# Performance work log

Measured on AMD Instinct MI355X. Metric: run time of the kernel, lower is better.

## Reference

```python
import jax, jax.numpy as jnp
import numpy as np

N, G, E, HD, H, L = 22528, 1024, 473088, 64, 4, 4
C = HD  # per-head out channels; concat=False -> mean over heads


def _ln(x, g, b, eps=1e-5):
    m = x.mean(-1, keepdims=True)
    v = ((x - m) ** 2).mean(-1, keepdims=True)
    return (x - m) * jax.lax.rsqrt(v + eps) * g + b


def setup_inputs() -> dict:
    key = jax.random.key(0)
    ks = iter(jax.random.split(key, 48))
    def rn(shape, s=0.1):
        return jax.random.normal(next(ks), shape, jnp.float32) * s
    inp = {}
    inp['x'] = jax.random.normal(next(ks), (N, 7), jnp.float32)
    inp['edge_index'] = jax.random.randint(next(ks), (2, E), 0, N)
    inp['edge_attr'] = jax.random.normal(next(ks), (E, 5), jnp.float32)
    inp['context'] = jax.random.normal(next(ks), (G, 3), jnp.float32)
    inp['batch'] = jnp.sort(jax.random.randint(next(ks), (N,), 0, G))
    inp['role'] = jax.random.randint(next(ks), (N,), 0, 5)
    inp['side'] = jax.random.randint(next(ks), (N,), 0, 3)
    inp['formation'] = jax.random.randint(next(ks), (G,), 0, 8)
    inp['alignment'] = jax.random.randint(next(ks), (G,), 0, 10)
    inp.update(
        W_emb=rn((7, HD)), b_emb=jnp.zeros((HD,)),
        role_table=rn((5, HD)), side_table=rn((3, HD // 2)),
        W_ctx=rn((3, HD)), b_ctx=jnp.zeros((HD,)),
        form_table=rn((8, HD)), align_table=rn((10, HD)),
        Wl=rn((L, HD, H * C)), bl=jnp.zeros((L, H * C)),
        Wr=rn((L, HD, H * C)), br=jnp.zeros((L, H * C)),
        We=rn((L, 5, H * C)), att=rn((L, H, C)), gat_bias=jnp.zeros((L, C)),
        ln_g=jnp.ones((L, HD)), ln_b=jnp.zeros((L, HD)),
        sp_W1=rn((2 * HD, HD)), sp_b1=jnp.zeros((HD,)),
        sp_W2=rn((HD, HD)), sp_b2=jnp.zeros((HD,)),
        sp_Wg=rn((HD, HD)), sp_bg=jnp.zeros((HD,)),
        fn_g=jnp.ones((HD,)), fn_b=jnp.zeros((HD,)),
    )
    return inp


def reference(x, edge_index, edge_attr, context, batch, role, side, formation, alignment,
              W_emb, b_emb, role_table, side_table, W_ctx, b_ctx, form_table, align_table,
              Wl, bl, Wr, br, We, att, gat_bias, ln_g, ln_b,
              sp_W1, sp_b1, sp_W2, sp_b2, sp_Wg, sp_bg, fn_g, fn_b):
    n = x.shape[0]
    # input embedding + categorical embedding fusion
    h = jax.nn.relu(x @ W_emb + b_emb)
    h = h + role_table[role]
    s = side_table[side]
    h = h + jnp.pad(s, ((0, 0), (0, h.shape[1] - s.shape[1])))
    c = jax.nn.relu(context @ W_ctx + b_ctx) + form_table[formation] + align_table[alignment]
    h = h + c[batch]
    src, dst = edge_index[0], edge_index[1]
    # PyG GATv2Conv default add_self_loops=True, fill_value='mean' for edge_attr
    deg_in = jax.ops.segment_sum(jnp.ones((src.shape[0], 1), h.dtype), dst, num_segments=n)
    self_attr = jax.ops.segment_sum(edge_attr, dst, num_segments=n) / jnp.maximum(deg_in, 1.0)
    loop = jnp.arange(n)
    src_a = jnp.concatenate([src, loop])
    dst_a = jnp.concatenate([dst, loop])
    ea = jnp.concatenate([edge_attr, self_attr], axis=0)
    for i in range(Wl.shape[0]):
        h_res = h
        x_l = (h @ Wl[i] + bl[i]).reshape(n, H, C)
        x_r = (h @ Wr[i] + br[i]).reshape(n, H, C)
        ee = (ea @ We[i]).reshape(-1, H, C)
        e = jax.nn.leaky_relu(x_l[src_a] + x_r[dst_a] + ee, 0.2)  # [E', H, C]
        logits = jnp.einsum('ehc,hc->eh', e, att[i])
        m = jax.lax.stop_gradient(jax.ops.segment_max(logits, dst_a, num_segments=n))
        p = jnp.exp(logits - m[dst_a])
        denom = jax.ops.segment_sum(p, dst_a, num_segments=n)
        alpha = p / denom[dst_a]  # softmax over incoming edges per head
        out = jax.ops.segment_sum(alpha[:, :, None] * x_l[src_a], dst_a, num_segments=n)
        out = out.mean(axis=1) + gat_bias[i]  # concat=False -> head mean + bias
        h = _ln(jax.nn.relu(out) + h_res, ln_g[i], ln_b[i])
    # social pooling: gated pairwise MLP, scatter-mean onto src
    pair = jnp.concatenate([h[src], h[dst]], axis=-1)
    inter = jax.nn.relu(pair @ sp_W1 + sp_b1) @ sp_W2 + sp_b2
    gated = inter * jax.nn.sigmoid(inter @ sp_Wg + sp_bg)
    cnt = jax.ops.segment_sum(jnp.ones((src.shape[0], 1), h.dtype), src, num_segments=n)
    pooled = jax.ops.segment_sum(gated, src, num_segments=n) / jnp.maximum(cnt, 1.0)
    h = h + pooled
    return _ln(h, fn_g, fn_b)
```

## Files before the change

kernel.cpp:

```cpp
#include <hip/hip_runtime.h>
#include <hip/hip_bf16.h>
#include <hip/hip_fp16.h>

#define N_NODES 22528
#define N_GRAPH 1024
#define N_EDGE  473088
#define HD 64

typedef unsigned short u16;
typedef unsigned int u32;
typedef unsigned char u8;
typedef __attribute__((ext_vector_type(8))) short bf16x8;
typedef __attribute__((ext_vector_type(4))) float f32x4;
typedef __attribute__((ext_vector_type(2))) float f32x2;
typedef __attribute__((ext_vector_type(4))) unsigned int u32x4;
typedef __attribute__((ext_vector_type(2))) _Float16 h2;
typedef __attribute__((ext_vector_type(2))) __fp16 fp16x2;
typedef __attribute__((ext_vector_type(8))) __fp16 fp16x8;

union FragU { bf16x8 v; u16 u[8]; u32 w[4]; };
union Frag16 { fp16x8 v; u16 u[8]; u32 w[4]; };
union HbU { uint4 v; u16 u[8]; };
union EaU { uint4 v; u32x4 e; u16 u[8]; u32 w[4]; };
union H2U { u32 w; h2 h; fp16x2 f; };

__device__ __forceinline__ float b2f(u16 u) {
    union { u32 i; float f; } v; v.i = ((u32)u) << 16; return v.f;
}
__device__ __forceinline__ float lo16(u32 w) {
    union { u32 i; float f; } v; v.i = w << 16; return v.f;
}
__device__ __forceinline__ float hi16(u32 w) {
    union { u32 i; float f; } v; v.i = w & 0xFFFF0000u; return v.f;
}
__device__ __forceinline__ u16 f2b(float f) {
    union { float f; u32 i; } v; v.f = f;
    u32 u = v.i;
    return (u16)((u + 0x7FFFu + ((u >> 16) & 1u)) >> 16);
}
__device__ __forceinline__ u16 f2h(float f) {
    union { __half h; u16 u; } c; c.h = __float2half(f); return c.u;
}
__device__ __forceinline__ float hlo(u32 w) {
    union { u16 u; __half h; } c; c.u = (u16)(w & 0xFFFFu); return __half2float(c.h);
}
__device__ __forceinline__ float hhi(u32 w) {
    union { u16 u; __half h; } c; c.u = (u16)(w >> 16); return __half2float(c.h);
}
__device__ __forceinline__ u8 f2fp8(float f) {
    return (u8)(__builtin_amdgcn_cvt_pk_fp8_f32(f, f, 0, false) & 0xFF);
}
__device__ __forceinline__ void dec8(u32 w, float* x) {
    f32x2 lo = __builtin_amdgcn_cvt_pk_f32_fp8((int)w, false);
    f32x2 hi = __builtin_amdgcn_cvt_pk_f32_fp8((int)w, true);
    x[0] = lo.x; x[1] = lo.y; x[2] = hi.x; x[3] = hi.y;
}
__device__ __forceinline__ int rdfl(u32 v) { return __builtin_amdgcn_readfirstlane((int)v); }
__device__ __forceinline__ h2 sblo(u32 w) { H2U c; c.w = (w & 0xFFFFu) | (w << 16); return c.h; }
__device__ __forceinline__ h2 sbhi(u32 w) { H2U c; c.w = (w >> 16) | (w & 0xFFFF0000u); return c.h; }
__device__ __forceinline__ h2 pkh(float a, float b) {
    H2U c; c.f = __builtin_amdgcn_cvt_pkrtz(a, b); return c.h;
}
__device__ __forceinline__ h2 u32h2(u32 w) { H2U c; c.w = w; return c.h; }
__device__ __forceinline__ u32 h2u32(h2 x) { H2U c; c.h = x; return c.w; }

#if __has_builtin(__builtin_amdgcn_fdot2)
__device__ __forceinline__ float FDOT2(h2 a, h2 b, float c) { return __builtin_amdgcn_fdot2(a, b, c, false); }
#else
__device__ __forceinline__ float FDOT2(h2 a, h2 b, float c) {
    return c + (float)a[0] * (float)b[0] + (float)a[1] * (float)b[1];
}
#endif

__device__ __forceinline__ float sum16(float v) {
    v += __int_as_float(__builtin_amdgcn_update_dpp(0, __float_as_int(v), 0x121, 0xF, 0xF, true));
    v += __int_as_float(__builtin_amdgcn_update_dpp(0, __float_as_int(v), 0x122, 0xF, 0xF, true));
    v += __int_as_float(__builtin_amdgcn_update_dpp(0, __float_as_int(v), 0x124, 0xF, 0xF, true));
    v += __int_as_float(__builtin_amdgcn_update_dpp(0, __float_as_int(v), 0x128, 0xF, 0xF, true));
    return v;
}

#define N_CVT 27
struct CvtTab { const void* src[N_CVT]; float* dst[N_CVT]; int n[N_CVT]; };

#define CPB 2048
#define NCHUNK (N_EDGE / CPB)
#define NRANGE 8
#define NPR (N_NODES / NRANGE)

__global__ __launch_bounds__(256) void k_count(const int* ei, int* ddst, int* dsrc,
                                               const void* ln_g, int* flag) {
    if (blockIdx.x == 0 && threadIdx.x == 0) {
        u32 w = ((const u32*)ln_g)[0];
        *flag = (w == 0x3F800000u) ? 1 : 0;
    }
    int r = blockIdx.x & 7;
    int c = blockIdx.x >> 3;
    int rlo = r * NPR, rhi = rlo + NPR;
    int base = c * CPB + threadIdx.x;
#pragma unroll
    for (int j = 0; j < CPB / 256; j++) {
        int e = base + j * 256;
        int s = __builtin_nontemporal_load(ei + e);
        int d = __builtin_nontemporal_load(ei + N_EDGE + e);
        if (d >= rlo && d < rhi) atomicAdd(&ddst[d], 1);
        if (s >= rlo && s < rhi) atomicAdd(&dsrc[s], 1);
    }
}

__global__ __launch_bounds__(256) void k_convert(CvtTab tab, const int* flagp) {
    int ty = blockIdx.y;
    const void* s = tab.src[ty];
    float* d = tab.dst[ty];
    int n = tab.n[ty];
    int f = *flagp;
    int stride = gridDim.x * 256;
    int i0 = blockIdx.x * 256 + threadIdx.x;
    if (f) {
        const float* sf = (const float*)s;
        for (int i = i0; i < n; i += stride) d[i] = sf[i];
    } else {
        const u16* sb = (const u16*)s;
        for (int i = i0; i < n; i += stride) d[i] = b2f(sb[i]);
    }
}

__global__ __launch_bounds__(256) void k_prepwlr(const float* Wl, const float* Wr, u16* wflr) {
    int idx = blockIdx.x * 256 + threadIdx.x;
    int f = idx >> 6, lane = idx & 63;
    int layer = f >> 6, lr = (f >> 5) & 1, ct = (f >> 1) & 15, kt = f & 1;
    const float* W = (lr ? Wr : Wl) + (size_t)layer * 64 * 256;
    int q = lane >> 4, m = lane & 15;
#pragma unroll
    for (int j = 0; j < 8; j++) {
        int k = kt * 32 + q * 8 + j;
        int nn = ct * 16 + m;
        wflr[(size_t)f * 512 + lane * 8 + j] = f2b(W[k * 256 + nn]);
    }
}

#define SCB 44
__global__ __launch_bounds__(512) void k_scanA(const int* ddst, const int* dsrc,
                                               int* pos_dst, int* pos_src,
                                               int* partial_d, int* partial_s) {
    __shared__ int wd[8], wss[8], wdx[8], wsx[8];
    int tid = threadIdx.x;
    int lane = tid & 63, wv = tid >> 6;
    int i = blockIdx.x * 512 + tid;
    int dd = ddst[i] + 1;
    int ds = dsrc[i];
    int sd = dd, ss = ds;
#pragma unroll
    for (int o = 1; o < 64; o <<= 1) {
        int t0 = __shfl_up(sd, o, 64);
        int t1 = __shfl_up(ss, o, 64);
        if (lane >= o) { sd += t0; ss += t1; }
    }
    if (lane == 63) { wd[wv] = sd; wss[wv] = ss; }
    __syncthreads();
    if (tid == 0) {
        int cd = 0, cs = 0;
#pragma unroll
        for (int w = 0; w < 8; w++) {
            int td = wd[w], ts = wss[w];
            wdx[w] = cd; wsx[w] = cs;
            cd += td; cs += ts;
        }
        partial_d[blockIdx.x] = cd;
        partial_s[blockIdx.x] = cs;
    }
    __syncthreads();
    pos_dst[i] = wdx[wv] + sd - dd;
    pos_src[i] = wsx[wv] + ss - ds;
}

__global__ __launch_bounds__(128) void k_scanB(int* partial_d, int* partial_s,
                                               int* off_dst, int* off_src) {
    int tid = threadIdx.x;
    int lane = tid & 63, wv = tid >> 6;
    int* arr = wv ? partial_s : partial_d;
    int v = (lane < SCB) ? arr[lane] : 0;
    int s = v;
#pragma unroll
    for (int o = 1; o < 64; o <<= 1) {
        int t = __shfl_up(s, o, 64);
        if (lane >= o) s += t;
    }
    if (lane < SCB) arr[lane] = s - v;
    if (lane == SCB - 1) {
        if (wv) off_src[N_NODES] = s;
        else    off_dst[N_NODES] = s;
    }
}

__global__ __launch_bounds__(512) void k_scanC(const int* partial_d, const int* partial_s,
                                               int* off_dst, int* pos_dst,
                                               int* off_src, int* pos_src,
                                               int* selfpos) {
    int i = blockIdx.x * 512 + threadIdx.x;
    int bd = partial_d[blockIdx.x];
    int bs = partial_s[blockIdx.x];
    int v = bd + pos_dst[i];
    off_dst[i] = v;
    selfpos[i] = v;
    pos_dst[i] = v + 1;
    int vs = bs + pos_src[i];
    off_src[i] = vs;
    pos_src[i] = vs;
}

__global__ __launch_bounds__(256) void k_scatter(const int* ei, const void* eattr_raw, const int* flagp,
                                                 int* pos_dst, int* pos_src,
                                                 u16* epermb, int* dstp) {
    int r = blockIdx.x & 7;
    int c = blockIdx.x >> 3;
    int rlo = r * NPR, rhi = rlo + NPR;
    int f = *flagp;
    int base = c * CPB + threadIdx.x;
#pragma unroll
    for (int j = 0; j < CPB / 256; j++) {
        int e = base + j * 256;
        int s = __builtin_nontemporal_load(ei + e);
        int d = __builtin_nontemporal_load(ei + N_EDGE + e);
        if (d >= rlo && d < rhi) {
            EaU b;
#pragma unroll
            for (int k = 0; k < 8; k++) b.u[k] = 0;
            if (f) {
                const float* sf = (const float*)eattr_raw;
#pragma unroll
                for (int k = 0; k < 5; k++) b.u[k] = f2h(__builtin_nontemporal_load(sf + (size_t)e * 5 + k));
            } else {
                const u16* sb = (const u16*)eattr_raw;
#pragma unroll
                for (int k = 0; k < 5; k++) b.u[k] = f2h(b2f(__builtin_nontemporal_load(sb + (size_t)e * 5 + k)));
            }
            b.w[3] = (u32)s;
            int slot = atomicAdd(&pos_dst[d], 1);
            ((u32x4*)epermb)[slot] = b.e;
        }
        if (s >= rlo && s < rhi) {
            int slot2 = atomicAdd(&pos_src[s], 1);
            dstp[slot2] = d;
        }
    }
}

__global__ __launch_bounds__(256) void k_selfattr(const int* off_dst, const int* selfpos, u16* epermb) {
    int lane = threadIdx.x & 63, wv = threadIdx.x >> 6;
    int q = lane >> 4, m15 = lane & 15;
    int n = blockIdx.x * 16 + wv * 4 + q;
    int slot = selfpos[n];
    int e0 = off_dst[n], e1 = off_dst[n + 1];
    float s0 = 0.f, s1 = 0.f, s2 = 0.f, s3 = 0.f, s4 = 0.f;
    for (int ii = e0 + m15; ii < e1; ii += 16) {
        if (ii == slot) continue;
        uint4 w = ((const uint4*)epermb)[ii];
        s0 += hlo(w.x); s1 += hhi(w.x); s2 += hlo(w.y); s3 += hhi(w.y); s4 += hlo(w.z);
    }
    s0 = sum16(s0); s1 = sum16(s1); s2 = sum16(s2); s3 = sum16(s3); s4 = sum16(s4);
    if (m15 == 0) {
        float inv = 1.f / fmaxf((float)(e1 - e0 - 1), 1.f);
        EaU b;
#pragma unroll
        for (int k = 0; k < 8; k++) b.u[k] = 0;
        b.u[0] = f2h(s0 * inv); b.u[1] = f2h(s1 * inv); b.u[2] = f2h(s2 * inv);
        b.u[3] = f2h(s3 * inv); b.u[4] = f2h(s4 * inv);
        b.w[3] = (u32)n;
        ((uint4*)epermb)[slot] = b.v;
    }
}

__global__ __launch_bounds__(256) void k_embed(const float* x, const float* W_emb, const float* b_emb,
                                               const int* role, const int* side, const int* batch,
                                               const float* role_t, const float* side_t,
                                               const float* context, const int* formation, const int* alignment,
                                               const float* W_ctx, const float* b_ctx,
                                               const float* form_t, const float* align_t,
                                               float* h) {
    int lane = threadIdx.x & 63, wv = threadIdx.x >> 6;
    int n = blockIdx.x * 4 + wv;
    float a = b_emb[lane];
#pragma unroll
    for (int k = 0; k < 7; k++) a += x[n * 7 + k] * W_emb[k * 64 + lane];
    a = fmaxf(a, 0.f);
    a += role_t[role[n] * 64 + lane];
    if (lane < 32) a += side_t[side[n] * 32 + lane];
    int g = batch[n];
    float c = b_ctx[lane];
#pragma unroll
    for (int k = 0; k < 3; k++) c += context[g * 3 + k] * W_ctx[k * 64 + lane];
    c = fmaxf(c, 0.f);
    c += form_t[formation[g] * 64 + lane] + align_t[alignment[g] * 64 + lane];
    h[n * 64 + lane] = a + c;
}

#define ATS 72

__global__ __launch_bounds__(256) void k_xlxr(const float* h, const u16* wflrL,
                                              const float* bl, const float* br, u8* xl8, u16* xrb) {
    __shared__ u16 hs[16 * ATS];
    int t = threadIdx.x;
    int n0 = blockIdx.x * 16;
#pragma unroll
    for (int r = 0; r < 4; r++) {
        int idx = t + r * 256;
        int m = idx >> 6, k = idx & 63;
        hs[m * ATS + k] = f2b(h[(size_t)(n0 + m) * 64 + k]);
    }
    __syncthreads();
    int lane = t & 63, wv = t >> 6;
    int q = lane >> 4, m15 = lane & 15;
    bf16x8 a0 = *(const bf16x8*)(hs + m15 * ATS + q * 8);
    bf16x8 a1 = *(const bf16x8*)(hs + m15 * ATS + 32 + q * 8);
#pragma unroll
    for (int lr = 0; lr < 2; lr++) {
        const float* bias = lr ? br : bl;
#pragma unroll
        for (int c4 = 0; c4 < 4; c4++) {
            int ct = wv * 4 + c4;
            const u16* fb = wflrL + (size_t)((lr * 16 + ct) * 2) * 512;
            f32x4 c = (f32x4){0.f, 0.f, 0.f, 0.f};
            c = __builtin_amdgcn_mfma_f32_16x16x32_bf16(a0, *(const bf16x8*)(fb + lane * 8), c, 0, 0, 0);
            c = __builtin_amdgcn_mfma_f32_16x16x32_bf16(a1, *(const bf16x8*)(fb + 512 + lane * 8), c, 0, 0, 0);
            float b = bias[ct * 16 + m15];
#pragma unroll
            for (int reg = 0; reg < 4; reg++) {
                int row = q * 4 + reg;
                float v = c[reg] + b;
                if (lr) xrb[(size_t)(n0 + row) * 256 + ct * 16 + m15] = f2b(v);
                else    xl8[(size_t)(n0 + row) * 256 + ct * 16 + m15] = f2fp8(v);
            }
        }
    }
}

__global__ __launch_bounds__(256) void k_gat(const u8* __restrict__ xl8, const u16* __restrict__ xrb,
                                             const uint4* __restrict__ epermb, const int* __restrict__ off_dst,
                                             const float* __restrict__ We, const float* __restrict__ att,
                                             const float* __restrict__ gat_bias,
                                             const float* __restrict__ ln_g, const float* __restrict__ ln_b,
                                             float* __restrict__ h) {
    __shared__ float lacc[2][2][4][64];
    __shared__ float lsum[2][2][4];
    int t = threadIdx.x;
    int lane = t & 63, wv = t >> 6;
    int nl = wv >> 1, half = wv & 1;
    int n = blockIdx.x * 2 + nl;
    int q = lane >> 4, m15 = lane & 15;
    float4 a4 = ((const float4*)att)[lane];
    h2 attP0 = pkh(a4.x, a4.y),               attP1 = pkh(a4.z, a4.w);
    h2 attN0 = pkh(0.2f * a4.x, 0.2f * a4.y), attN1 = pkh(0.2f * a4.z, 0.2f * a4.w);
    h2 weh[5][2];
#pragma unroll
    for (int k = 0; k < 5; k++) {
        float4 w4 = ((const float4*)(We + k * 256))[lane];
        weh[k][0] = pkh(w4.x, w4.y);
        weh[k][1] = pkh(w4.z, w4.w);
    }
    ushort4 xrp = ((const ushort4*)xrb)[(size_t)n * 64 + lane];
    h2 xrh0 = pkh(b2f(xrp.x), b2f(xrp.y));
    h2 xrh1 = pkh(b2f(xrp.z), b2f(xrp.w));
    const h2 hz = {(_Float16)0.f, (_Float16)0.f};
    int e0 = rdfl((u32)off_dst[n]);
    int e1 = rdfl((u32)off_dst[n + 1]);
    int mid = e0 + ((e1 - e0 + 1) >> 1);
    int a0 = half ? mid : e0;
    int a1 = half ? e1 : mid;
    float s_own = 0.f;
    float acc[4] = {0.f, 0.f, 0.f, 0.f};
    const u32* xl32 = (const u32*)xl8;
    int ii = a0;
    for (; ii + 2 <= a1; ii += 2) {
        uint4 ew0 = epermb[ii];
        uint4 ew1 = epermb[ii + 1];
        int s0 = rdfl(ew0.w);
        int s1 = rdfl(ew1.w);
        u32 xw0 = xl32[(size_t)s0 * 64 + lane];
        u32 xw1 = xl32[(size_t)s1 * 64 + lane];
        u32 e0x = (u32)rdfl(ew0.x), e0y = (u32)rdfl(ew0.y), e0z = (u32)rdfl(ew0.z);
        u32 e1x = (u32)rdfl(ew1.x), e1y = (u32)rdfl(ew1.y), e1z = (u32)rdfl(ew1.z);
        h2 eA0 = sblo(e0x), eA1 = sbhi(e0x), eA2 = sblo(e0y), eA3 = sbhi(e0y), eA4 = sblo(e0z);
        h2 eB0 = sblo(e1x), eB1 = sbhi(e1x), eB2 = sblo(e1y), eB3 = sbhi(e1y), eB4 = sblo(e1z);
        float xlf0[4], xlf1[4];
        dec8(xw0, xlf0);
        dec8(xw1, xlf1);
        h2 x0a = pkh(xlf0[0], xlf0[1]), x0b = pkh(xlf0[2], xlf0[3]);
        h2 x1a = pkh(xlf1[0], xlf1[1]), x1b = pkh(xlf1[2], xlf1[3]);
        h2 v0a = x0a + xrh0;
        h2 v0b = x0b + xrh1;
        h2 v1a = x1a + xrh0;
        h2 v1b = x1b + xrh1;
        v0a += eA0 * weh[0][0]; v0b += eA0 * weh[0][1];
        v0a += eA1 * weh[1][0]; v0b += eA1 * weh[1][1];
        v0a += eA2 * weh[2][0]; v0b += eA2 * weh[2][1];
        v0a += eA3 * weh[3][0]; v0b += eA3 * weh[3][1];
        v0a += eA4 * weh[4][0]; v0b += eA4 * weh[4][1];
        h2 p0a = __builtin_elementwise_max(v0a, hz), m0a = __builtin_elementwise_min(v0a, hz);
        h2 p0b = __builtin_elementwise_max(v0b, hz), m0b = __builtin_elementwise_min(v0b, hz);
        h2 p1a = __builtin_elementwise_max(v1a, hz), m1a = __builtin_elementwise_min(v1a, hz);
        h2 p1b = __builtin_elementwise_max(v1b, hz), m1b = __builtin_elementwise_min(v1b, hz);
        float lp0 = FDOT2(p0a, attP0, 0.f);
        lp0 = FDOT2(m0a, attN0, lp0);
        lp0 = FDOT2(p0b, attP1, lp0);
        lp0 = FDOT2(m0b, attN1, lp0);
        float lp1 = FDOT2(p1a, attP0, 0.f);
        lp1 = FDOT2(m1a, attN0, lp1);
        lp1 = FDOT2(p1b, attP1, lp1);
        lp1 = FDOT2(m1b, attN1, lp1);
        lp0 = sum16(lp0);
        lp1 = sum16(lp1);
        float p0 = __expf(fminf(lp0, 50.f));
        float p1 = __expf(fminf(lp1, 50.f));
        s_own += p0 + p1;
        acc[0] += p0 * xlf0[0] + p1 * xlf1[0];
        acc[1] += p0 * xlf0[1] + p1 * xlf1[1];
        acc[2] += p0 * xlf0[2] + p1 * xlf1[2];
        acc[3] += p0 * xlf0[3] + p1 * xlf1[3];
    }
    if (ii < a1) {
        uint4 ew = epermb[ii];
        int s0 = rdfl(ew.w);
        u32 xw = xl32[(size_t)s0 * 64 + lane];
        u32 ex = (u32)rdfl(ew.x), ey = (u32)rdfl(ew.y), ez = (u32)rdfl(ew.z);
        h2 eA0 = sblo(ex), eA1 = sbhi(ex), eA2 = sblo(ey), eA3 = sbhi(ey), eA4 = sblo(ez);
        float xlf[4];
        dec8(xw, xlf);
        h2 xa = pkh(xlf[0], xlf[1]), xb = pkh(xlf[2], xlf[3]);
        h2 va = xa + xrh0;
        h2 vb = xb + xrh1;
        va += eA0 * weh[0][0]; vb += eA0 * weh[0][1];
        va += eA1 * weh[1][0]; vb += eA1 * weh[1][1];
        va += eA2 * weh[2][0]; vb += eA2 * weh[2][1];
        va += eA3 * weh[3][0]; vb += eA3 * weh[3][1];
        va += eA4 * weh[4][0]; vb += eA4 * weh[4][1];
        h2 pa = __builtin_elementwise_max(va, hz), ma = __builtin_elementwise_min(va, hz);
        h2 pb = __builtin_elementwise_max(vb, hz), mb = __builtin_elementwise_min(vb, hz);
        float lp = FDOT2(pa, attP0, 0.f);
        lp = FDOT2(ma, attN0, lp);
        lp = FDOT2(pb, attP1, lp);
        lp = FDOT2(mb, attN1, lp);
        lp = sum16(lp);
        float p = __expf(fminf(lp, 50.f));
        s_own += p;
        acc[0] += p * xlf[0]; acc[1] += p * xlf[1];
        acc[2] += p * xlf[2]; acc[3] += p * xlf[3];
    }
    *(float4*)&lacc[nl][half][q][m15 * 4] = make_float4(acc[0], acc[1], acc[2], acc[3]);
    if (m15 == 0) lsum[nl][half][q] = s_own;
    __syncthreads();
    if (half == 0) {
        float o = 0.f;
#pragma unroll
        for (int j = 0; j < 4; j++) {
            float sj = lsum[nl][0][j] + lsum[nl][1][j];
            float aj = lacc[nl][0][j][lane] + lacc[nl][1][j][lane];
            o += aj / sj;
        }
        o = 0.25f * o + gat_bias[lane];
        float r = fmaxf(o, 0.f) + h[(size_t)n * 64 + lane];
        float mu = r;
#pragma unroll
        for (int mask = 1; mask < 64; mask <<= 1) mu += __shfl_xor(mu, mask, 64);
        mu *= (1.f / 64.f);
        float d = r - mu;
        float var = d * d;
#pragma unroll
        for (int mask = 1; mask < 64; mask <<= 1) var += __shfl_xor(var, mask, 64);
        var *= (1.f / 64.f);
        h[(size_t)n * 64 + lane] = d * rsqrtf(var + 1e-5f) * ln_g[lane] + ln_b[lane];
    }
}

__global__ __launch_bounds__(256) void k_poolprep(const float* h, const float* W1, const float* sp_b1,
                                                  u16* hA, u16* hBb,
                                                  const float* W2, const float* Wg, u16* wfrag) {
    int t = threadIdx.x;
    if (blockIdx.x == N_NODES / 8) {
#pragma unroll
        for (int r = 0; r < 4; r++) {
            int i = t + r * 256;
            int frag = i >> 6, lane = i & 63;
            const float* W = (frag < 8) ? W2 : Wg;
            int f = frag & 7;
            int ct = f >> 1, kt = f & 1;
#pragma unroll
            for (int j = 0; j < 8; j++) {
                int k = kt * 32 + (lane >> 4) * 8 + j;
                int nn = ct * 16 + (lane & 15);
                wfrag[i * 8 + j] = f2h(W[k * 64 + nn]);
            }
        }
        return;
    }
    __shared__ float hs[512];
    int n0 = blockIdx.x * 8;
    hs[t] = h[n0 * 64 + t];
    hs[t + 256] = h[n0 * 64 + 256 + t];
    __syncthreads();
    int c = t & 63;
    int half = (t >> 6) & 1;
    int jg = t >> 7;
    const float* w = W1 + half * 4096;
    float acc[4] = {0.f, 0.f, 0.f, 0.f};
    for (int k = 0; k < 64; k++) {
        float wv_ = w[k * 64 + c];
#pragma unroll
        for (int j = 0; j < 4; j++) acc[j] += hs[(jg * 4 + j) * 64 + k] * wv_;
    }
    float b1 = sp_b1[c];
#pragma unroll
    for (int j = 0; j < 4; j++) {
        int n = n0 + jg * 4 + j;
        if (half) hBb[(size_t)n * 64 + c] = f2h(acc[j]);
        else      hA[(size_t)n * 64 + c] = f2h(acc[j] + b1);
    }
}

#define TBS 72

__global__ __launch_bounds__(256) void k_pool(const float* h, const u16* hA, const u16* hBb,
                                              const int* dstp, const int* off_src, const u16* wfrag,
                                              const float* sp_b2, const float* sp_bg,
                                              const float* fn_g, const float* fn_b,
                                              void* outv, const int* flagp) {
    __shared__ u16 smem[8192 + 4 * 16 * TBS];
    int t = threadIdx.x;
#pragma unroll
    for (int r = 0; r < 4; r++)
        ((uint4*)smem)[t + r * 256] = ((const uint4*)wfrag)[t + r * 256];
    __syncthreads();
    int lane = t & 63, wv = t >> 6;
    int n = blockIdx.x * 4 + wv;
    int q = lane >> 4, m15 = lane & 15;
    u16* tb = smem + 8192 + wv * 16 * TBS;

    const uint4* hap = (const uint4*)(hA + (size_t)n * 64);
    uint4 ha0r = hap[q], ha1r = hap[4 + q];
    h2 ha0h[4] = {u32h2(ha0r.x), u32h2(ha0r.y), u32h2(ha0r.z), u32h2(ha0r.w)};
    h2 ha1h[4] = {u32h2(ha1r.x), u32h2(ha1r.y), u32h2(ha1r.z), u32h2(ha1r.w)};
    const h2 hz = {(_Float16)0.f, (_Float16)0.f};
    float b2r[4], bgr[4];
#pragma unroll
    for (int ct = 0; ct < 4; ct++) {
        b2r[ct] = sp_b2[ct * 16 + m15];
        bgr[ct] = sp_bg[ct * 16 + m15];
    }
    f32x4 pacc[4];
#pragma unroll
    for (int ct = 0; ct < 4; ct++) pacc[ct] = (f32x4){0.f, 0.f, 0.f, 0.f};

    int e0 = off_src[n], e1 = off_src[n + 1];
    int deg = e1 - e0;
    for (int base = e0; base < e1; base += 16) {
        int slot = base + m15;
        int ec = (slot < e1) ? slot : (e1 - 1);
        int dst = dstp[ec];
        const uint4* hbp = (const uint4*)(hBb + (size_t)dst * 64);
        uint4 hb0 = hbp[q], hb1 = hbp[4 + q];
        Frag16 A0, A1;
        A0.w[0] = h2u32(__builtin_elementwise_max(ha0h[0] + u32h2(hb0.x), hz));
        A0.w[1] = h2u32(__builtin_elementwise_max(ha0h[1] + u32h2(hb0.y), hz));
        A0.w[2] = h2u32(__builtin_elementwise_max(ha0h[2] + u32h2(hb0.z), hz));
        A0.w[3] = h2u32(__builtin_elementwise_max(ha0h[3] + u32h2(hb0.w), hz));
        A1.w[0] = h2u32(__builtin_elementwise_max(ha1h[0] + u32h2(hb1.x), hz));
        A1.w[1] = h2u32(__builtin_elementwise_max(ha1h[1] + u32h2(hb1.y), hz));
        A1.w[2] = h2u32(__builtin_elementwise_max(ha1h[2] + u32h2(hb1.z), hz));
        A1.w[3] = h2u32(__builtin_elementwise_max(ha1h[3] + u32h2(hb1.w), hz));
        f32x4 c2[4];
#pragma unroll
        for (int ct = 0; ct < 4; ct++) {
            f32x4 c = (f32x4){0.f, 0.f, 0.f, 0.f};
            c = __builtin_amdgcn_mfma_f32_16x16x32_f16(A0.v, *(const fp16x8*)(smem + (ct * 2 + 0) * 512 + lane * 8), c, 0, 0, 0);
            c = __builtin_amdgcn_mfma_f32_16x16x32_f16(A1.v, *(const fp16x8*)(smem + (ct * 2 + 1) * 512 + lane * 8), c, 0, 0, 0);
#pragma unroll
            for (int reg = 0; reg < 4; reg++) c[reg] += b2r[ct];
            c2[ct] = c;
        }
#pragma unroll
        for (int ct = 0; ct < 4; ct++)
#pragma unroll
            for (int reg = 0; reg < 4; reg++)
                tb[(q * 4 + reg) * TBS + ct * 16 + m15] = f2h(c2[ct][reg]);
        __asm__ volatile("s_waitcnt lgkmcnt(0)" ::: "memory");
        Frag16 A2_0, A2_1;
        A2_0.v = *(const fp16x8*)(tb + m15 * TBS + q * 8);
        A2_1.v = *(const fp16x8*)(tb + m15 * TBS + 32 + q * 8);
#pragma unroll
        for (int ct = 0; ct < 4; ct++) {
            f32x4 c = (f32x4){0.f, 0.f, 0.f, 0.f};
            c = __builtin_amdgcn_mfma_f32_16x16x32_f16(A2_0.v, *(const fp16x8*)(smem + 4096 + (ct * 2 + 0) * 512 + lane * 8), c, 0, 0, 0);
            c = __builtin_amdgcn_mfma_f32_16x16x32_f16(A2_1.v, *(const fp16x8*)(smem + 4096 + (ct * 2 + 1) * 512 + lane * 8), c, 0, 0, 0);
#pragma unroll
            for (int reg = 0; reg < 4; reg++) {
                float tgv = c[reg] + bgr[ct];
                float gv = c2[ct][reg] * (1.f / (1.f + __expf(-tgv)));
                int row = q * 4 + reg;
                pacc[ct][reg] += ((base + row) < e1) ? gv : 0.f;
            }
        }
    }
    float psum[4];
#pragma unroll
    for (int ct = 0; ct < 4; ct++) {
        psum[ct] = (pacc[ct][0] + pacc[ct][1]) + (pacc[ct][2] + pacc[ct][3]);
        psum[ct] += __shfl_xor(psum[ct], 16, 64);
        psum[ct] += __shfl_xor(psum[ct], 32, 64);
    }
    float pooled = (q == 0) ? psum[0] : (q == 1) ? psum[1] : (q == 2) ? psum[2] : psum[3];
    float r = h[n * 64 + lane] + pooled / fmaxf((float)deg, 1.f);
    float mu = r;
#pragma unroll
    for (int mask = 1; mask < 64; mask <<= 1) mu += __shfl_xor(mu, mask, 64);
    mu *= (1.f / 64.f);
    float d = r - mu;
    float var = d * d;
#pragma unroll
    for (int mask = 1; mask < 64; mask <<= 1) var += __shfl_xor(var, mask, 64);
    var *= (1.f / 64.f);
    float res = d * rsqrtf(var + 1e-5f) * fn_g[lane] + fn_b[lane];
    if (*flagp) ((float*)outv)[n * 64 + lane] = res;
    else        ((u16*)outv)[n * 64 + lane] = f2b(res);
}

extern "C" void kernel_launch(void* const* d_in, const int* in_sizes, int n_in,
                              void* d_out, int out_size, void* d_ws, size_t ws_size,
                              hipStream_t stream) {
    const int* ei       = (const int*)d_in[1];
    const int* batch    = (const int*)d_in[4];
    const int* role     = (const int*)d_in[5];
    const int* side     = (const int*)d_in[6];
    const int* formation= (const int*)d_in[7];
    const int* alignment= (const int*)d_in[8];

    const int cvt_idx[N_CVT] = {0,3, 9,10,11,12,13,14,15,16, 17,18,19,20,21,22,23,24,25, 26,27,28,29,30,31,32,33};
    const int cvt_n[N_CVT] = {
        N_NODES*7, N_GRAPH*3,
        7*64, 64, 5*64, 3*32, 3*64, 64, 8*64, 10*64,
        4*64*256, 4*256, 4*64*256, 4*256, 4*5*256, 4*4*64, 4*64, 4*64, 4*64,
        128*64, 64, 64*64, 64, 64*64, 64, 64, 64
    };

    float* ws = (float*)d_ws;
    size_t off = 0;
    CvtTab tab;
    float* cv[N_CVT];
    for (int i = 0; i < N_CVT; i++) {
        tab.src[i] = d_in[cvt_idx[i]];
        tab.dst[i] = ws + off;
        tab.n[i]   = cvt_n[i];
        cv[i] = ws + off;
        off += cvt_n[i];
    }
    const float* x      = cv[0];
    const float* context= cv[1];
    const float* W_emb  = cv[2];
    const float* b_emb  = cv[3];
    const float* role_t = cv[4];
    const float* side_t = cv[5];
    const float* W_ctx  = cv[6];
    const float* b_ctx  = cv[7];
    const float* form_t = cv[8];
    const float* align_t= cv[9];
    const float* Wl     = cv[10];
    const float* bl     = cv[11];
    const float* Wr     = cv[12];
    const float* br     = cv[13];
    const float* We     = cv[14];
    const float* att    = cv[15];
    const float* gat_bias = cv[16];
    const float* ln_g   = cv[17];
    const float* ln_b   = cv[18];
    const float* sp_W1  = cv[19];
    const float* sp_b1  = cv[20];
    const float* sp_W2  = cv[21];
    const float* sp_b2  = cv[22];
    const float* sp_Wg  = cv[23];
    const float* sp_bg  = cv[24];
    const float* fn_g   = cv[25];
    const float* fn_b   = cv[26];

    float* h   = ws + off; off += (size_t)N_NODES * 64;
    u8*   xl8  = (u8*)(ws + off); off += (size_t)N_NODES * 64;
    u16*  xrb  = (u16*)(ws + off); off += (size_t)N_NODES * 128;
    u16*  hA   = (u16*)(ws + off); off += (size_t)N_NODES * 32;
    u16*  hBb  = (u16*)(ws + off); off += (size_t)N_NODES * 32;
    u16*  wfrag= (u16*)(ws + off); off += 4096;
    u16*  wflr = (u16*)(ws + off); off += 65536;
    u16*  epermb = (u16*)(ws + off); off += (size_t)(N_EDGE + N_NODES) * 4;
    int* dstp = (int*)(ws + off); off += (size_t)N_EDGE;
    int* ddst = (int*)(ws + off); off += N_NODES;
    int* dsrc = (int*)(ws + off); off += N_NODES;
    int* off_dst = (int*)(ws + off); off += N_NODES + 1;
    int* pos_dst = (int*)(ws + off); off += N_NODES;
    int* off_src = (int*)(ws + off); off += N_NODES + 1;
    int* pos_src = (int*)(ws + off); off += N_NODES;
    int* selfpos = (int*)(ws + off); off += N_NODES;
    int* flagp   = (int*)(ws + off); off += 1;
    int* partial_d = (int*)(ws + off); off += SCB;
    int* partial_s = (int*)(ws + off); off += SCB;

    hipMemsetAsync(ddst, 0, 2 * N_NODES * sizeof(int), stream);
    k_count<<<NCHUNK * NRANGE, 256, 0, stream>>>(ei, ddst, dsrc, d_in[24], flagp);
    k_convert<<<dim3(64, N_CVT), 256, 0, stream>>>(tab, flagp);
    k_prepwlr<<<64, 256, 0, stream>>>(Wl, Wr, wflr);
    k_scanA<<<SCB, 512, 0, stream>>>(ddst, dsrc, pos_dst, pos_src, partial_d, partial_s);
    k_scanB<<<1, 128, 0, stream>>>(partial_d, partial_s, off_dst, off_src);
    k_scanC<<<SCB, 512, 0, stream>>>(partial_d, partial_s, off_dst, pos_dst,
                                     off_src, pos_src, selfpos);
    k_scatter<<<NCHUNK * NRANGE, 256, 0, stream>>>(ei, d_in[2], flagp, pos_dst, pos_src,
                                                   epermb, dstp);
    k_selfattr<<<N_NODES / 16, 256, 0, stream>>>(off_dst, selfpos, epermb);
    k_embed<<<N_NODES / 4, 256, 0, stream>>>(x, W_emb, b_emb, role, side, batch, role_t, side_t,
                                             context, formation, alignment, W_ctx, b_ctx,
                                             form_t, align_t, h);
    for (int i = 0; i < 4; i++) {
        k_xlxr<<<N_NODES / 16, 256, 0, stream>>>(h, wflr + (size_t)i * 32768,
                                                 bl + (size_t)i * 256, br + (size_t)i * 256, xl8, xrb);
        k_gat<<<N_NODES / 2, 256, 0, stream>>>(xl8, xrb, (const uint4*)epermb, off_dst,
                                               We + (size_t)i * 5 * 256, att + (size_t)i * 256,
                                               gat_bias + (size_t)i * 64,
                                               ln_g + (size_t)i * 64, ln_b + (size_t)i * 64, h);
    }
    k_poolprep<<<N_NODES / 8 + 1, 256, 0, stream>>>(h, sp_W1, sp_b1, hA, hBb, sp_W2, sp_Wg, wfrag);
    k_pool<<<N_NODES / 4, 256, 0, stream>>>(h, hA, hBb, dstp, off_src, wfrag,
                                            sp_b2, sp_bg, fn_g, fn_b, d_out, flagp);
}
```

Before: 545.6 us.

## Assign one wavefront per node in GAT kernel and halve edge-range passes

```diff
diff --git a/kernel.cpp b/kernel.cpp
--- a/kernel.cpp
+++ b/kernel.cpp
@@ -85,7 +85,7 @@
 
 #define CPB 2048
 #define NCHUNK (N_EDGE / CPB)
-#define NRANGE 8
+#define NRANGE 4
 #define NPR (N_NODES / NRANGE)
 
 __global__ __launch_bounds__(256) void k_count(const int* ei, int* ddst, int* dsrc,
@@ -94,8 +94,8 @@
         u32 w = ((const u32*)ln_g)[0];
         *flag = (w == 0x3F800000u) ? 1 : 0;
     }
-    int r = blockIdx.x & 7;
-    int c = blockIdx.x >> 3;
+    int r = blockIdx.x & (NRANGE - 1);
+    int c = blockIdx.x >> 2;
     int rlo = r * NPR, rhi = rlo + NPR;
     int base = c * CPB + threadIdx.x;
 #pragma unroll
@@ -212,8 +212,8 @@
 __global__ __launch_bounds__(256) void k_scatter(const int* ei, const void* eattr_raw, const int* flagp,
                                                  int* pos_dst, int* pos_src,
                                                  u16* epermb, int* dstp) {
-    int r = blockIdx.x & 7;
-    int c = blockIdx.x >> 3;
+    int r = blockIdx.x & (NRANGE - 1);
+    int c = blockIdx.x >> 2;
     int rlo = r * NPR, rhi = rlo + NPR;
     int f = *flagp;
     int base = c * CPB + threadIdx.x;
@@ -341,12 +341,10 @@
                                              const float* __restrict__ gat_bias,
                                              const float* __restrict__ ln_g, const float* __restrict__ ln_b,
                                              float* __restrict__ h) {
-    __shared__ float lacc[2][2][4][64];
-    __shared__ float lsum[2][2][4];
+    __shared__ float lacc[4][4][64];
     int t = threadIdx.x;
     int lane = t & 63, wv = t >> 6;
-    int nl = wv >> 1, half = wv & 1;
-    int n = blockIdx.x * 2 + nl;
+    int n = blockIdx.x * 4 + wv;
     int q = lane >> 4, m15 = lane & 15;
     float4 a4 = ((const float4*)att)[lane];
     h2 attP0 = pkh(a4.x, a4.y),               attP1 = pkh(a4.z, a4.w);
@@ -362,11 +360,8 @@
     h2 xrh0 = pkh(b2f(xrp.x), b2f(xrp.y));
     h2 xrh1 = pkh(b2f(xrp.z), b2f(xrp.w));
     const h2 hz = {(_Float16)0.f, (_Float16)0.f};
-    int e0 = rdfl((u32)off_dst[n]);
-    int e1 = rdfl((u32)off_dst[n + 1]);
-    int mid = e0 + ((e1 - e0 + 1) >> 1);
-    int a0 = half ? mid : e0;
-    int a1 = half ? e1 : mid;
+    int a0 = rdfl((u32)off_dst[n]);
+    int a1 = rdfl((u32)off_dst[n + 1]);
     float s_own = 0.f;
     float acc[4] = {0.f, 0.f, 0.f, 0.f};
     const u32* xl32 = (const u32*)xl8;
@@ -396,6 +391,11 @@
         v0a += eA2 * weh[2][0]; v0b += eA2 * weh[2][1];
         v0a += eA3 * weh[3][0]; v0b += eA3 * weh[3][1];
         v0a += eA4 * weh[4][0]; v0b += eA4 * weh[4][1];
+        v1a += eB0 * weh[0][0]; v1b += eB0 * weh[0][1];
+        v1a += eB1 * weh[1][0]; v1b += eB1 * weh[1][1];
+        v1a += eB2 * weh[2][0]; v1b += eB2 * weh[2][1];
+        v1a += eB3 * weh[3][0]; v1b += eB3 * weh[3][1];
+        v1a += eB4 * weh[4][0]; v1b += eB4 * weh[4][1];
         h2 p0a = __builtin_elementwise_max(v0a, hz), m0a = __builtin_elementwise_min(v0a, hz);
         h2 p0b = __builtin_elementwise_max(v0b, hz), m0b = __builtin_elementwise_min(v0b, hz);
         h2 p1a = __builtin_elementwise_max(v1a, hz), m1a = __builtin_elementwise_min(v1a, hz);
@@ -446,30 +446,26 @@
         acc[0] += p * xlf[0]; acc[1] += p * xlf[1];
         acc[2] += p * xlf[2]; acc[3] += p * xlf[3];
     }
-    *(float4*)&lacc[nl][half][q][m15 * 4] = make_float4(acc[0], acc[1], acc[2], acc[3]);
-    if (m15 == 0) lsum[nl][half][q] = s_own;
-    __syncthreads();
-    if (half == 0) {
-        float o = 0.f;
-#pragma unroll
-        for (int j = 0; j < 4; j++) {
-            float sj = lsum[nl][0][j] + lsum[nl][1][j];
-            float aj = lacc[nl][0][j][lane] + lacc[nl][1][j][lane];
-            o += aj / sj;
-        }
-        o = 0.25f * o + gat_bias[lane];
-        float r = fmaxf(o, 0.f) + h[(size_t)n * 64 + lane];
-        float mu = r;
-#pragma unroll
-        for (int mask = 1; mask < 64; mask <<= 1) mu += __shfl_xor(mu, mask, 64);
-        mu *= (1.f / 64.f);
-        float d = r - mu;
-        float var = d * d;
-#pragma unroll
-        for (int mask = 1; mask < 64; mask <<= 1) var += __shfl_xor(var, mask, 64);
-        var *= (1.f / 64.f);
-        h[(size_t)n * 64 + lane] = d * rsqrtf(var + 1e-5f) * ln_g[lane] + ln_b[lane];
-    }
+    *(float4*)&lacc[wv][q][m15 * 4] = make_float4(acc[0], acc[1], acc[2], acc[3]);
+    __asm__ volatile("s_waitcnt lgkmcnt(0)" ::: "memory");
+    float o = 0.f;
+#pragma unroll
+    for (int j = 0; j < 4; j++) {
+        float sj = __shfl(s_own, j * 16, 64);
+        o += lacc[wv][j][lane] / sj;
+    }
+    o = 0.25f * o + gat_bias[lane];
+    float r = fmaxf(o, 0.f) + h[(size_t)n * 64 + lane];
+    float mu = r;
+#pragma unroll
+    for (int mask = 1; mask < 64; mask <<= 1) mu += __shfl_xor(mu, mask, 64);
+    mu *= (1.f / 64.f);
+    float d = r - mu;
+    float var = d * d;
+#pragma unroll
+    for (int mask = 1; mask < 64; mask <<= 1) var += __shfl_xor(var, mask, 64);
+    var *= (1.f / 64.f);
+    h[(size_t)n * 64 + lane] = d * rsqrtf(var + 1e-5f) * ln_g[lane] + ln_b[lane];
 }
 
 __global__ __launch_bounds__(256) void k_poolprep(const float* h, const float* W1, const float* sp_b1,
@@ -717,7 +713,7 @@
     for (int i = 0; i < 4; i++) {
         k_xlxr<<<N_NODES / 16, 256, 0, stream>>>(h, wflr + (size_t)i * 32768,
                                                  bl + (size_t)i * 256, br + (size_t)i * 256, xl8, xrb);
-        k_gat<<<N_NODES / 2, 256, 0, stream>>>(xl8, xrb, (const uint4*)epermb, off_dst,
+        k_gat<<<N_NODES / 4, 256, 0, stream>>>(xl8, xrb, (const uint4*)epermb, off_dst,
                                                We + (size_t)i * 5 * 256, att + (size_t)i * 256,
                                                gat_bias + (size_t)i * 64,
                                                ln_g + (size_t)i * 64, ln_b + (size_t)i * 64, h);
```

Measured after the change: 532.7 us. -2.4%, faster.
